# Optimization experiments

Hardware: AMD Instinct MI355X
Metric: run time of the kernel (lower is better)

Reference implementation:

```python
import jax, jax.numpy as jnp
import numpy as np

N_HEADS = 16
HEAD_SIZE = 64

def setup_inputs() -> dict:
    key = jax.random.key(0)
    k1, k2 = jax.random.split(key)
    B, N, D = 2, 2048, N_HEADS * HEAD_SIZE
    x = jax.random.normal(k1, (B, N, D), dtype=jnp.float32)
    # lecun_normal-ish scale for the QKV kernel
    W_qkv = jax.random.normal(k2, (D, 3 * D), dtype=jnp.float32) * (1.0 / np.sqrt(D))
    return {"x": x, "W_qkv": W_qkv}

def reference(x, W_qkv):
    B, N, D = x.shape
    H, Dh = N_HEADS, HEAD_SIZE
    qkv = x @ W_qkv                                  # [B,N,3D]
    q, k, v = jnp.split(qkv, 3, axis=-1)
    q = q.reshape(B, N, H, Dh)
    k = k.reshape(B, N, H, Dh)
    v = v.reshape(B, N, H, Dh)
    dist = jnp.einsum('bihd,bjhd->bhij', q, k) / jnp.sqrt(jnp.asarray(Dh, dtype=x.dtype))
    mask = jnp.tril(jnp.ones((N, N), dtype=bool))[None, None, :, :]
    dist = jnp.where(mask, dist, -jnp.inf)
    attn = jax.nn.softmax(dist, axis=-1)             # [B,H,N,N]
    out_heads = jnp.einsum('bhij,bjhd->bihd', attn, v)
    return out_heads.reshape(B, N, H * Dh)
```

## Files before the change

kernel.cpp:

```cpp
#include <hip/hip_runtime.h>

typedef __attribute__((ext_vector_type(8))) short bf16x8;
typedef __attribute__((ext_vector_type(4))) float f32x4;
typedef __attribute__((ext_vector_type(16))) float f32x16;
typedef __attribute__((ext_vector_type(2))) unsigned int u32x2;

#define DEVI static __device__ __forceinline__

namespace {
constexpr int NSEQ = 2048, NH = 16;
constexpr int D = 1024, D3 = 3072;
}

DEVI unsigned short f2bf(float f) {
  union { float f; unsigned int u; } v; v.f = f;
  unsigned int r = v.u + 0x7FFFu + ((v.u >> 16) & 1u);
  return (unsigned short)(r >> 16);
}

DEVI void gload16(const unsigned short* g, unsigned short* lds_) {
  __builtin_amdgcn_global_load_lds(
      (const __attribute__((address_space(1))) unsigned int*)g,
      (__attribute__((address_space(3))) unsigned int*)lds_, 16, 0, 0);
}

DEVI f32x4 mfma16(bf16x8 a, bf16x8 b, f32x4 c) {
  return __builtin_amdgcn_mfma_f32_16x16x32_bf16(a, b, c, 0, 0, 0);
}

DEVI f32x16 mfma32(bf16x8 a, bf16x8 b, f32x16 c) {
  return __builtin_amdgcn_mfma_f32_32x32x16_bf16(a, b, c, 0, 0, 0);
}

DEVI float exp2g(float x) {
#if __has_builtin(__builtin_amdgcn_exp2f)
  return __builtin_amdgcn_exp2f(x);
#else
  return exp2f(x);
#endif
}

DEVI unsigned int cvtpk(float a, float b) {
  unsigned int r;
  asm("v_cvt_pk_bf16_f32 %0, %1, %2" : "=v"(r) : "v"(a), "v"(b));
  return r;
}

DEVI u32x2 pswap2(unsigned int a, unsigned int b) {
  return __builtin_amdgcn_permlane32_swap(a, b, false, false);
}
DEVI float xmax_halves(float v) {
  union { float f; unsigned int u; } c; c.f = v;
  u32x2 r = pswap2(c.u, c.u);
  union { unsigned int u; float f; } x, y; x.u = r.x; y.u = r.y;
  return fmaxf(x.f, y.f);
}

union U4 { unsigned int u[4]; bf16x8 v; };

__global__ __launch_bounds__(256) void prep_k(const float* __restrict__ x,
                                              const float* __restrict__ W,
                                              unsigned short* __restrict__ xb,
                                              unsigned short* __restrict__ Wt) {
  __shared__ float t[32][33];
  const int bid = blockIdx.x;
  if (bid < 4096) {
    int i = (bid * 256 + threadIdx.x) * 4;
    float4 v = *reinterpret_cast<const float4*>(x + i);
    ushort4 o;
    o.x = f2bf(v.x); o.y = f2bf(v.y); o.z = f2bf(v.z); o.w = f2bf(v.w);
    *reinterpret_cast<ushort4*>(xb + i) = o;
  } else {
    const int b2 = bid - 4096;
    const int c0 = (b2 % 96) * 32, k0 = (b2 / 96) * 32;
    const int tx = threadIdx.x & 31, ty = threadIdx.x >> 5;
#pragma unroll
    for (int r = 0; r < 32; r += 8)
      t[ty + r][tx] = W[(size_t)(k0 + ty + r) * D3 + c0 + tx];
    __syncthreads();
#pragma unroll
    for (int r = 0; r < 32; r += 8)
      Wt[(size_t)(c0 + ty + r) * D + k0 + tx] = f2bf(t[tx][ty + r]);
  }
}

__global__ __launch_bounds__(256) void qkv_gemm_k(const unsigned short* __restrict__ xb,
                                                  const unsigned short* __restrict__ Wt,
                                                  unsigned short* __restrict__ qw,
                                                  unsigned short* __restrict__ kw,
                                                  unsigned short* __restrict__ vtw) {
  __shared__ unsigned short smA[128 * 32];
  __shared__ unsigned short smB[128 * 32];
  const int tid = threadIdx.x, w = tid >> 6, l = tid & 63;
  const int m0 = blockIdx.x * 128, n0 = blockIdx.y * 128;
  const int wm = w >> 1, wn = w & 1;

  const unsigned short* ga[2]; const unsigned short* gb[2];
  unsigned short* la[2]; unsigned short* lb[2];
#pragma unroll
  for (int i = 0; i < 2; ++i) {
    int idx = tid + i * 256;
    int row = idx >> 2;
    int blk = (idx & 3) ^ ((row >> 1) & 3);
    ga[i] = xb + (size_t)(m0 + row) * D + blk * 8;
    gb[i] = Wt + (size_t)(n0 + row) * D + blk * 8;
    la[i] = smA + (w * 64 + i * 256) * 8;
    lb[i] = smB + (w * 64 + i * 256) * 8;
  }

  f32x4 acc[4][4];
#pragma unroll
  for (int a = 0; a < 4; ++a)
#pragma unroll
    for (int b = 0; b < 4; ++b) acc[a][b] = (f32x4){0.f, 0.f, 0.f, 0.f};

  for (int kt = 0; kt < D / 32; ++kt) {
    __syncthreads();
#pragma unroll
    for (int i = 0; i < 2; ++i) {
      gload16(ga[i] + kt * 32, la[i]);
      gload16(gb[i] + kt * 32, lb[i]);
    }
    asm volatile("s_waitcnt vmcnt(0)" ::: "memory");
    __syncthreads();

    bf16x8 af[4], bfr[4];
#pragma unroll
    for (int a = 0; a < 4; ++a) {
      int arow = wm * 64 + a * 16 + (l & 15);
      int blk = (l >> 4) ^ ((arow >> 1) & 3);
      af[a] = *reinterpret_cast<const bf16x8*>(smA + arow * 32 + blk * 8);
    }
#pragma unroll
    for (int b = 0; b < 4; ++b) {
      int brow = wn * 64 + b * 16 + (l & 15);
      int blk = (l >> 4) ^ ((brow >> 1) & 3);
      bfr[b] = *reinterpret_cast<const bf16x8*>(smB + brow * 32 + blk * 8);
    }
#pragma unroll
    for (int a = 0; a < 4; ++a)
#pragma unroll
      for (int b = 0; b < 4; ++b)
        acc[a][b] = mfma16(af[a], bfr[b], acc[a][b]);
  }

  const int which = n0 >> 10;
#pragma unroll
  for (int a = 0; a < 4; ++a) {
#pragma unroll
    for (int b = 0; b < 4; ++b) {
#pragma unroll
      for (int r = 0; r < 4; ++r) {
        int grow = m0 + wm * 64 + a * 16 + (l >> 4) * 4 + r;
        int gcol = n0 + wn * 64 + b * 16 + (l & 15);
        float v = acc[a][b][r];
        int bb = grow >> 11, n = grow & 2047;
        int cc = gcol & 1023, h = cc >> 6, dh = cc & 63;
        size_t bh = (size_t)bb * NH + h;
        if (which == 0)
          qw[(bh * NSEQ + n) * 64 + dh] = f2bf(v * 0.18033688011112042f);
        else if (which == 1)
          kw[(bh * NSEQ + n) * 64 + dh] = f2bf(v);
        else
          vtw[(bh * 64 + dh) * NSEQ + n] = f2bf(v);
      }
    }
  }
}

__global__ __launch_bounds__(256, 2) void attn_k(const unsigned short* __restrict__ qw,
                                                 const unsigned short* __restrict__ kw,
                                                 const unsigned short* __restrict__ vtw,
                                                 float* __restrict__ out) {
  __shared__ __align__(16) char lds[66560];
  const int tid = threadIdx.x, w = tid >> 6, l = tid & 63;
  const int hi = l >> 5, ql = l & 31;
  const int qsub = w >> 1, par = w & 1;

  const int wg = blockIdx.x;
  const int xcd = wg & 7, rest = wg >> 3;
  const int bhl = rest >> 4;
  const int j = rest & 15;
  const int bh = xcd * 4 + bhl;
  const int bb = bh >> 4, h = bh & 15;

  const unsigned short* qb = qw + (size_t)bh * NSEQ * 64;
  const unsigned short* kb = kw + (size_t)bh * NSEQ * 64;
  const unsigned short* vb = vtw + (size_t)bh * 64 * NSEQ;

  const int r0 = tid >> 3, c0 = (tid & 7) ^ (r0 & 7);
  const int r1 = (tid + 256) >> 3, c1 = ((tid + 256) & 7) ^ (r1 & 7);
  const int wbase = w * 512;

#define STAGE(SL, PR)                                                            \
  do {                                                                           \
    const int t0_ = 2 * (PR), t1_ = 2 * (PR) + 1;                                \
    unsigned short* k0d = (unsigned short*)(lds + (SL) * 32768) + wbase;         \
    unsigned short* v0d = (unsigned short*)(lds + (SL) * 32768 + 8192) + wbase;  \
    unsigned short* k1d = (unsigned short*)(lds + (SL) * 32768 + 16384) + wbase; \
    unsigned short* v1d = (unsigned short*)(lds + (SL) * 32768 + 24576) + wbase; \
    gload16(kb + (((size_t)t0_ * 64 + r0) * 64 + c0 * 8), k0d);                  \
    gload16(kb + (((size_t)t0_ * 64 + r1) * 64 + c1 * 8), k0d + 2048);           \
    gload16(vb + ((size_t)r0 * NSEQ + t0_ * 64 + c0 * 8), v0d);                  \
    gload16(vb + ((size_t)r1 * NSEQ + t0_ * 64 + c1 * 8), v0d + 2048);           \
    gload16(kb + (((size_t)t1_ * 64 + r0) * 64 + c0 * 8), k1d);                  \
    gload16(kb + (((size_t)t1_ * 64 + r1) * 64 + c1 * 8), k1d + 2048);           \
    gload16(vb + ((size_t)r0 * NSEQ + t1_ * 64 + c0 * 8), v1d);                  \
    gload16(vb + ((size_t)r1 * NSEQ + t1_ * 64 + c1 * 8), v1d + 2048);           \
  } while (0)

  for (int seg = 0; seg < 2; ++seg) {
    const int qt = seg ? j : (31 - j);
    const int qbase = qt * 64;
    const int qg = qbase + qsub * 32 + ql;

    bf16x8 qf[4];
#pragma unroll
    for (int ds = 0; ds < 4; ++ds)
      qf[ds] = *reinterpret_cast<const bf16x8*>(qb + (size_t)qg * 64 + ds * 16 + hi * 8);

    float m = -1e30f, lsum = 0.f;
    f32x16 O0, O1;
#pragma unroll
    for (int r2 = 0; r2 < 16; ++r2) { O0[r2] = 0.f; O1[r2] = 0.f; }

    const int nsup = (qt >> 1) + 1;
    STAGE(0, 0);
    for (int s = 0; s < nsup; ++s) {
      __syncthreads();
      if (s + 1 < nsup) STAGE((s + 1) & 1, s + 1);
      const int t = 2 * s + par;
      if (t <= qt) {
        const char* Kb = lds + (s & 1) * 32768 + par * 16384;
        const char* Vb = Kb + 8192;

        f32x16 S0, S1;
#pragma unroll
        for (int r2 = 0; r2 < 16; ++r2) { S0[r2] = 0.f; S1[r2] = 0.f; }
        __builtin_amdgcn_s_setprio(1);
#pragma unroll
        for (int ds = 0; ds < 4; ++ds) {
          bf16x8 k0 = *reinterpret_cast<const bf16x8*>(
              Kb + ql * 128 + (((2 * ds + hi) ^ (ql & 7)) << 4));
          bf16x8 k1 = *reinterpret_cast<const bf16x8*>(
              Kb + (32 + ql) * 128 + (((2 * ds + hi) ^ (ql & 7)) << 4));
          S0 = mfma32(k0, qf[ds], S0);
          S1 = mfma32(k1, qf[ds], S1);
        }
        __builtin_amdgcn_s_setprio(0);

        if (t == qt) {
#pragma unroll
          for (int reg = 0; reg < 16; ++reg) {
            const int krow = (reg & 3) + 8 * (reg >> 2) + 4 * hi;
            if (64 * t + krow > qg) S0[reg] = -1e30f;
            if (64 * t + 32 + krow > qg) S1[reg] = -1e30f;
          }
        }

        float t0 = fmaxf(S0[0], S1[0]), t1 = fmaxf(S0[1], S1[1]);
        float t2 = fmaxf(S0[2], S1[2]), t3 = fmaxf(S0[3], S1[3]);
#pragma unroll
        for (int r2 = 4; r2 < 16; r2 += 4) {
          t0 = fmaxf(t0, fmaxf(S0[r2], S1[r2]));
          t1 = fmaxf(t1, fmaxf(S0[r2 + 1], S1[r2 + 1]));
          t2 = fmaxf(t2, fmaxf(S0[r2 + 2], S1[r2 + 2]));
          t3 = fmaxf(t3, fmaxf(S0[r2 + 3], S1[r2 + 3]));
        }
        float tmax = xmax_halves(fmaxf(fmaxf(t0, t1), fmaxf(t2, t3)));

        if (!__all(tmax <= m + 8.0f)) {
          const float mn = fmaxf(m, tmax);
          const float g = exp2g(m - mn);
          m = mn;
          lsum *= g;
#pragma unroll
          for (int r2 = 0; r2 < 16; ++r2) { O0[r2] *= g; O1[r2] *= g; }
        }

        float pr0[16], pr1[16];
        float rA = 0.f, rB = 0.f, rC = 0.f, rD = 0.f;
#pragma unroll
        for (int r2 = 0; r2 < 16; r2 += 4) {
          pr0[r2] = exp2g(S0[r2] - m);     pr1[r2] = exp2g(S1[r2] - m);
          pr0[r2 + 1] = exp2g(S0[r2 + 1] - m); pr1[r2 + 1] = exp2g(S1[r2 + 1] - m);
          pr0[r2 + 2] = exp2g(S0[r2 + 2] - m); pr1[r2 + 2] = exp2g(S1[r2 + 2] - m);
          pr0[r2 + 3] = exp2g(S0[r2 + 3] - m); pr1[r2 + 3] = exp2g(S1[r2 + 3] - m);
          rA += pr0[r2] + pr1[r2];
          rB += pr0[r2 + 1] + pr1[r2 + 1];
          rC += pr0[r2 + 2] + pr1[r2 + 2];
          rD += pr0[r2 + 3] + pr1[r2 + 3];
        }
        {
          float rsum = (rA + rB) + (rC + rD);
          union { float f; unsigned int u; } c; c.f = rsum;
          u32x2 r = pswap2(c.u, c.u);
          union { unsigned int u; float f; } x, y; x.u = r.x; y.u = r.y;
          lsum += x.f + y.f;
        }

        bf16x8 pf[4];
#pragma unroll
        for (int ct = 0; ct < 2; ++ct) {
          const float* pp = ct ? pr1 : pr0;
          unsigned int u[4][2];
#pragma unroll
          for (int c = 0; c < 4; ++c) {
            u[c][0] = cvtpk(pp[4 * c], pp[4 * c + 1]);
            u[c][1] = cvtpk(pp[4 * c + 2], pp[4 * c + 3]);
          }
#pragma unroll
          for (int kk = 0; kk < 2; ++kk) {
            u32x2 rw0 = pswap2(u[2 * kk][0], u[2 * kk + 1][0]);
            u32x2 rw1 = pswap2(u[2 * kk][1], u[2 * kk + 1][1]);
            U4 f;
            f.u[0] = rw0.x; f.u[1] = rw1.x;
            f.u[2] = rw0.y; f.u[3] = rw1.y;
            pf[2 * ct + kk] = f.v;
          }
        }

        __builtin_amdgcn_s_setprio(1);
#pragma unroll
        for (int ks = 0; ks < 4; ++ks) {
          bf16x8 v0 = *reinterpret_cast<const bf16x8*>(
              Vb + ql * 128 + (((2 * ks + hi) ^ (ql & 7)) << 4));
          bf16x8 v1 = *reinterpret_cast<const bf16x8*>(
              Vb + (32 + ql) * 128 + (((2 * ks + hi) ^ (ql & 7)) << 4));
          O0 = mfma32(v0, pf[ks], O0);
          O1 = mfma32(v1, pf[ks], O1);
        }
        __builtin_amdgcn_s_setprio(0);
      }
    }

    __syncthreads();
    float* mlp = (float*)(lds + 65536);
    if (l < 32) { mlp[w * 64 + l] = m; mlp[w * 64 + 32 + l] = lsum; }
    __syncthreads();
    {
      const int pw = w ^ 1;
      const float m1 = mlp[pw * 64 + ql];
      const float l1 = mlp[pw * 64 + 32 + ql];
      const float M = fmaxf(m, m1);
      const float g0 = exp2g(m - M);
      const float g1 = exp2g(m1 - M);
      const float L = lsum * g0 + l1 * g1;
      const float phi = g0 / L;
      float* mo = (float*)lds + (qsub * 2 + par) * 2048;
#pragma unroll
      for (int reg = 0; reg < 16; ++reg) {
        const int dr = (reg & 3) + 8 * (reg >> 2) + 4 * hi;
        const int d1 = 32 + dr;
        mo[ql * 64 + (((dr >> 2) ^ (ql & 7)) << 2) + (dr & 3)] = O0[reg] * phi;
        mo[ql * 64 + (((d1 >> 2) ^ (ql & 7)) << 2) + (d1 & 3)] = O1[reg] * phi;
      }
    }
    __syncthreads();
    {
      const int qq = tid >> 2, dq = (tid & 3) << 4;
      const float* pa = (float*)lds + ((qq >> 5) * 2 + 0) * 2048 + (qq & 31) * 64;
      const float* pb = (float*)lds + ((qq >> 5) * 2 + 1) * 2048 + (qq & 31) * 64;
      float* op = out + ((size_t)bb * NSEQ + qbase + qq) * D + h * 64 + dq;
#pragma unroll
      for (int c = 0; c < 4; ++c) {
        const int ch = ((dq >> 2) + c) ^ (qq & 7);
        float4 va = *reinterpret_cast<const float4*>(pa + ch * 4);
        float4 vb4 = *reinterpret_cast<const float4*>(pb + ch * 4);
        float4 s4 = make_float4(va.x + vb4.x, va.y + vb4.y, va.z + vb4.z, va.w + vb4.w);
        *reinterpret_cast<float4*>(op + c * 4) = s4;
      }
    }
    __syncthreads();
  }
#undef STAGE
}

extern "C" void kernel_launch(void* const* d_in, const int* in_sizes, int n_in,
                              void* d_out, int out_size, void* d_ws, size_t ws_size,
                              hipStream_t stream) {
  const float* x = (const float*)d_in[0];
  const float* W = (const float*)d_in[1];
  float* out = (float*)d_out;
  char* ws = (char*)d_ws;
  unsigned short* xb  = (unsigned short*)(ws);
  unsigned short* Wt  = (unsigned short*)(ws + 8388608);
  unsigned short* qw  = (unsigned short*)(ws + 14680064);
  unsigned short* kw  = (unsigned short*)(ws + 23068672);
  unsigned short* vtw = (unsigned short*)(ws + 31457280);

  prep_k<<<7168, 256, 0, stream>>>(x, W, xb, Wt);
  qkv_gemm_k<<<dim3(32, 24), 256, 0, stream>>>(xb, Wt, qw, kw, vtw);
  attn_k<<<512, 256, 0, stream>>>(qw, kw, vtw, out);
}
```

Before: 85.12 us.

## Remap QKV GEMM tiles per XCD and stage V transpose through LDS

Switches the QKV GEMM to a 1D grid and remaps block IDs so each XCD works on a compact 16x6 patch of output tiles, improving L2 reuse of A and B panels. For the V portion, the scattered strided bf16 stores into the transposed V buffer are replaced by one warp at a time staging its 64x64 tile in LDS, then writing 16-byte coalesced rows. This adds extra barriers and serialises the four warps during the V epilogue.

```diff
diff --git a/kernel.cpp b/kernel.cpp
--- a/kernel.cpp
+++ b/kernel.cpp
@@ -89,10 +89,15 @@
                                                   unsigned short* __restrict__ qw,
                                                   unsigned short* __restrict__ kw,
                                                   unsigned short* __restrict__ vtw) {
-  __shared__ unsigned short smA[128 * 32];
-  __shared__ unsigned short smB[128 * 32];
+  __shared__ unsigned short shm[8192];
+  unsigned short* smA = shm;
+  unsigned short* smB = shm + 4096;
   const int tid = threadIdx.x, w = tid >> 6, l = tid & 63;
-  const int m0 = blockIdx.x * 128, n0 = blockIdx.y * 128;
+  const int bid = blockIdx.x;
+  const int xcd = bid & 7, cc2 = bid >> 3;
+  const int mt = (xcd & 1) * 16 + (cc2 & 15);
+  const int nt = (xcd >> 1) * 6 + (cc2 >> 4);
+  const int m0 = mt * 128, n0 = nt * 128;
   const int wm = w >> 1, wn = w & 1;
 
   const unsigned short* ga[2]; const unsigned short* gb[2];
@@ -145,24 +150,56 @@
   }
 
   const int which = n0 >> 10;
-#pragma unroll
-  for (int a = 0; a < 4; ++a) {
-#pragma unroll
-    for (int b = 0; b < 4; ++b) {
-#pragma unroll
-      for (int r = 0; r < 4; ++r) {
-        int grow = m0 + wm * 64 + a * 16 + (l >> 4) * 4 + r;
-        int gcol = n0 + wn * 64 + b * 16 + (l & 15);
-        float v = acc[a][b][r];
-        int bb = grow >> 11, n = grow & 2047;
-        int cc = gcol & 1023, h = cc >> 6, dh = cc & 63;
-        size_t bh = (size_t)bb * NH + h;
-        if (which == 0)
-          qw[(bh * NSEQ + n) * 64 + dh] = f2bf(v * 0.18033688011112042f);
-        else if (which == 1)
-          kw[(bh * NSEQ + n) * 64 + dh] = f2bf(v);
-        else
-          vtw[(bh * 64 + dh) * NSEQ + n] = f2bf(v);
+  if (which != 2) {
+#pragma unroll
+    for (int a = 0; a < 4; ++a) {
+#pragma unroll
+      for (int b = 0; b < 4; ++b) {
+#pragma unroll
+        for (int r = 0; r < 4; ++r) {
+          int grow = m0 + wm * 64 + a * 16 + (l >> 4) * 4 + r;
+          int gcol = n0 + wn * 64 + b * 16 + (l & 15);
+          float v = acc[a][b][r];
+          int bb = grow >> 11, n = grow & 2047;
+          int cc = gcol & 1023, h = cc >> 6, dh = cc & 63;
+          size_t bh = (size_t)bb * NH + h;
+          if (which == 0)
+            qw[(bh * NSEQ + n) * 64 + dh] = f2bf(v * 0.18033688011112042f);
+          else
+            kw[(bh * NSEQ + n) * 64 + dh] = f2bf(v);
+        }
+      }
+    }
+  } else {
+    const int nb = m0 + wm * 64;
+    const int bbv = nb >> 11;
+    const int nloc = nb & 2047;
+    const int gc = n0 + wn * 64;
+    const int hh = (gc & 1023) >> 6;
+    unsigned short* vtb = vtw + ((size_t)bbv * NH + hh) * 64 * NSEQ;
+    for (int pw = 0; pw < 4; ++pw) {
+      __syncthreads();
+      if (w == pw) {
+#pragma unroll
+        for (int a = 0; a < 4; ++a) {
+#pragma unroll
+          for (int b = 0; b < 4; ++b) {
+            const int dh = b * 16 + (l & 15);
+            const int nn = a * 16 + ((l >> 4) << 2);
+            ushort4 pk;
+            pk.x = f2bf(acc[a][b][0]);
+            pk.y = f2bf(acc[a][b][1]);
+            pk.z = f2bf(acc[a][b][2]);
+            pk.w = f2bf(acc[a][b][3]);
+            *reinterpret_cast<ushort4*>(shm + dh * 68 + nn) = pk;
+          }
+        }
+#pragma unroll
+        for (int p = 0; p < 8; ++p) {
+          const int dh = p * 8 + (l >> 3);
+          bf16x8 v = *reinterpret_cast<const bf16x8*>(shm + dh * 68 + ((l & 7) << 3));
+          *reinterpret_cast<bf16x8*>(vtb + (size_t)dh * NSEQ + nloc + ((l & 7) << 3)) = v;
+        }
       }
     }
   }
@@ -390,6 +427,6 @@
   unsigned short* vtw = (unsigned short*)(ws + 31457280);
 
   prep_k<<<7168, 256, 0, stream>>>(x, W, xb, Wt);
-  qkv_gemm_k<<<dim3(32, 24), 256, 0, stream>>>(xb, Wt, qw, kw, vtw);
+  qkv_gemm_k<<<768, 256, 0, stream>>>(xb, Wt, qw, kw, vtw);
   attn_k<<<512, 256, 0, stream>>>(qw, kw, vtw, out);
 }
```

Result: slower. 91.05 us (+7.0%).
